# Kernel optimization log

Hardware: AMD Instinct MI355X
Metric: run time of the kernel (lower is better)

The kernel has to match this reference:

```python
import jax, jax.numpy as jnp
import numpy as np
from jax import lax

BN_EPS = 1e-5

def dwconv(x, w, dilation):
    # x: [N,C,H,W], w: [C,1,k,k] depthwise; SAME padding = (r*(k-1)+1)//2
    k = w.shape[-1]
    pad = (dilation * (k - 1) + 1) // 2
    return lax.conv_general_dilated(
        x, w, window_strides=(1, 1), padding=[(pad, pad), (pad, pad)],
        rhs_dilation=(dilation, dilation), feature_group_count=x.shape[1],
        dimension_numbers=('NCHW', 'OIHW', 'NCHW'))

def bn_eval(y, gamma, beta, mean, var):
    # inference BatchNorm2d over channel dim; params: [C]
    inv = gamma * lax.rsqrt(var + BN_EPS)
    return y * inv[None, :, None, None] + (beta - mean * inv)[None, :, None, None]

def setup_inputs() -> dict:
    key = jax.random.key(0)
    ks = jax.random.split(key, 13)
    C = 384
    x = jax.random.normal(ks[0], (16, C, 56, 56), jnp.float32)
    w_lk = jax.random.normal(ks[1], (C, 1, 13, 13), jnp.float32) * 0.05
    w_b0 = jax.random.normal(ks[2], (C, 1, 5, 5), jnp.float32) * 0.05
    w_b1 = jax.random.normal(ks[3], (C, 1, 7, 7), jnp.float32) * 0.05
    w_b2 = jax.random.normal(ks[4], (C, 1, 7, 7), jnp.float32) * 0.05
    w_b3 = jax.random.normal(ks[5], (C, 1, 3, 3), jnp.float32) * 0.05
    w_b4 = jax.random.normal(ks[6], (C, 1, 3, 3), jnp.float32) * 0.05
    w_b5 = jax.random.normal(ks[7], (C, 1, 3, 3), jnp.float32) * 0.05
    bn_gamma = jax.random.uniform(ks[8], (7, C), jnp.float32, 0.5, 1.5)
    bn_beta = jax.random.normal(ks[9], (7, C), jnp.float32) * 0.1
    bn_mean = jax.random.normal(ks[10], (7, C), jnp.float32) * 0.1
    bn_var = jax.random.uniform(ks[11], (7, C), jnp.float32, 0.5, 1.5)
    return dict(x=x, w_lk=w_lk, w_b0=w_b0, w_b1=w_b1, w_b2=w_b2, w_b3=w_b3,
                w_b4=w_b4, w_b5=w_b5, bn_gamma=bn_gamma, bn_beta=bn_beta,
                bn_mean=bn_mean, bn_var=bn_var)

def reference(x, w_lk, w_b0, w_b1, w_b2, w_b3, w_b4, w_b5,
              bn_gamma, bn_beta, bn_mean, bn_var):
    # DilatedReparamBlock (kernel_size=13, non-deploy):
    # out = BN(dw13(x)) + sum_i BN_i(dw_{k_i, r_i}(x))
    dilates = (1, 1, 2, 3, 4, 5)
    branch_ws = (w_b0, w_b1, w_b2, w_b3, w_b4, w_b5)
    out = bn_eval(dwconv(x, w_lk, 1), bn_gamma[0], bn_beta[0], bn_mean[0], bn_var[0])
    for i, (w, r) in enumerate(zip(branch_ws, dilates)):
        j = i + 1
        out = out + bn_eval(dwconv(x, w, r), bn_gamma[j], bn_beta[j], bn_mean[j], bn_var[j])
    return out
```

## Files before the change

### kernel.cpp

```cpp
#include <hip/hip_runtime.h>
#include <hip/hip_fp16.h>


#define CCH 384
#define SP 56
#define PWH 72
#define NPLANES (16*384)

typedef __attribute__((ext_vector_type(4))) unsigned int u32x4;
typedef _Float16 hf2 __attribute__((ext_vector_type(2)));

__device__ __forceinline__ float rfl(float v) {
    return __int_as_float(__builtin_amdgcn_readfirstlane(__float_as_int(v)));
}
__device__ __forceinline__ unsigned rflu(unsigned v) {
    return (unsigned)__builtin_amdgcn_readfirstlane((int)v);
}
__device__ __forceinline__ hf2 as_hf2(unsigned v) {
    union { unsigned u; hf2 h; } x; x.u = v; return x.h;
}
__device__ __forceinline__ float dot2h(float c, unsigned x, unsigned w) {
#if __has_builtin(__builtin_amdgcn_fdot2)
    return __builtin_amdgcn_fdot2(as_hf2(x), as_hf2(w), c, false);
#else
    hf2 xh = as_hf2(x), wh = as_hf2(w);
    return fmaf((float)xh.x, (float)wh.x, fmaf((float)xh.y, (float)wh.y, c));
#endif
}

__global__ __launch_bounds__(64, 2) void drb_conv13_r14(
    const float* __restrict__ x,
    const float* __restrict__ w_lk, const float* __restrict__ w_b0,
    const float* __restrict__ w_b1, const float* __restrict__ w_b2,
    const float* __restrict__ w_b3, const float* __restrict__ w_b4,
    const float* __restrict__ w_b5,
    const float* __restrict__ gamma, const float* __restrict__ beta,
    const float* __restrict__ mean, const float* __restrict__ var,
    float* __restrict__ out)
{
    __shared__ __align__(16) __half sxh[68 * PWH];
    __shared__ __align__(16) float sw[13 * 16];
    __shared__ __align__(16) unsigned swh[13 * 8];

    const int plane = blockIdx.x;
    const int c = plane % CCH;
    const int tid = threadIdx.x;
    const float* __restrict__ xp = x + (size_t)plane * (SP * SP);

    float4 stage[13];
    #pragma unroll
    for (int k = 0; k < 13; k++) {
        int i4 = tid + 64 * k;
        if (i4 < SP * SP / 4) stage[k] = ((const float4*)xp)[i4];
    }

    float S[7];
    float bias = 0.f;
    #pragma unroll
    for (int j = 0; j < 7; j++) {
        float inv = gamma[j * CCH + c] * rsqrtf(var[j * CCH + c] + 1e-5f);
        S[j] = inv;
        bias += beta[j * CCH + c] - mean[j * CCH + c] * inv;
    }

    {
        u32x4 z = {0u, 0u, 0u, 0u};
        #pragma unroll
        for (int k = 0; k < 10; k++) {
            int i = tid + 64 * k;
            if (i < (68 * PWH) / 8) ((u32x4*)sxh)[i] = z;
        }
    }

    #pragma unroll
    for (int k = 0; k < 4; k++) {
        int t = tid + 64 * k;
        if (t < 13 * 16) {
            int ky = t >> 4, kx = t & 15;
            float w = 0.f;
            if (kx < 13) {
                w = S[0] * w_lk[c * 169 + ky * 13 + kx];
                if (ky >= 4 && ky <= 8 && kx >= 4 && kx <= 8)
                    w += S[1] * w_b0[c * 25 + (ky - 4) * 5 + (kx - 4)];
                if (ky >= 3 && ky <= 9 && kx >= 3 && kx <= 9)
                    w += S[2] * w_b1[c * 49 + (ky - 3) * 7 + (kx - 3)];
                if (!(ky & 1) && !(kx & 1))
                    w += S[3] * w_b2[c * 49 + (ky >> 1) * 7 + (kx >> 1)];
                if (ky >= 3 && ky <= 9 && (ky - 3) % 3 == 0 &&
                    kx >= 3 && kx <= 9 && (kx - 3) % 3 == 0)
                    w += S[4] * w_b3[c * 9 + ((ky - 3) / 3) * 3 + (kx - 3) / 3];
                if (ky >= 2 && ky <= 10 && (ky - 2) % 4 == 0 &&
                    kx >= 2 && kx <= 10 && (kx - 2) % 4 == 0)
                    w += S[5] * w_b4[c * 9 + ((ky - 2) / 4) * 3 + (kx - 2) / 4];
                if (ky >= 1 && ky <= 11 && (ky - 1) % 5 == 0 &&
                    kx >= 1 && kx <= 11 && (kx - 1) % 5 == 0)
                    w += S[6] * w_b5[c * 9 + ((ky - 1) / 5) * 3 + (kx - 1) / 5];
            }
            sw[t] = w;
        }
    }

    #pragma unroll
    for (int k = 0; k < 2; k++) {
        int t = tid + 64 * k;
        if (t < 13 * 8) {
            int ky = t >> 3, p = t & 7;
            float w0 = sw[ky * 16 + 2 * p];
            float w1 = sw[ky * 16 + 2 * p + 1];
            hf2 hh; hh.x = (_Float16)w0; hh.y = (_Float16)w1;
            union { hf2 h; unsigned u; } cv; cv.h = hh;
            swh[t] = cv.u;
        }
    }

    #pragma unroll
    for (int k = 0; k < 13; k++) {
        int i4 = tid + 64 * k;
        if (i4 < SP * SP / 4) {
            float4 v = stage[k];
            int r = i4 / 14;
            int col = (i4 - r * 14) * 4;
            __half2* d2 = (__half2*)&sxh[(r + 6) * PWH + col + 8];
            d2[0] = __floats2half2_rn(v.x, v.y);
            d2[1] = __floats2half2_rn(v.z, v.w);
        }
    }
    __syncthreads();

    const int xg = tid & 7;
    const int yg = tid >> 3;
    const int xgc = (xg < 7) ? xg : 3;
    const int Yb = yg * 7;
    const __half* __restrict__ sbaseh = &sxh[Yb * PWH + 8 * xgc];

    float acc[7][8];
    #pragma unroll
    for (int r = 0; r < 7; r++)
        #pragma unroll
        for (int j = 0; j < 8; j++) acc[r][j] = 0.f;

#define ROWDOT(ROWP, DYN, WPA)                                              \
    {                                                                       \
        const u32x4* cp_ = (const u32x4*)(ROWP);                            \
        u32x4 c0_ = cp_[0], c1_ = cp_[1], c2_ = cp_[2];                     \
        unsigned e_[12], o_[11];                                            \
        e_[0]=c0_.x; e_[1]=c0_.y; e_[2]=c0_.z; e_[3]=c0_.w;                 \
        e_[4]=c1_.x; e_[5]=c1_.y; e_[6]=c1_.z; e_[7]=c1_.w;                 \
        e_[8]=c2_.x; e_[9]=c2_.y; e_[10]=c2_.z; e_[11]=c2_.w;               \
        _Pragma("unroll")                                                   \
        for (int t_ = 1; t_ <= 10; t_++)                                    \
            o_[t_] = (e_[t_] >> 16) | (e_[t_ + 1] << 16);                   \
        _Pragma("unroll")                                                   \
        for (int dy_ = 0; dy_ < (DYN); dy_++) {                             \
            const int r_ = i - dy_ - RBASE;                                 \
            if (r_ >= 0 && r_ < 7) {                                        \
                _Pragma("unroll")                                           \
                for (int j_ = 0; j_ < 8; j_++) {                            \
                    float a_ = acc[r_][j_];                                 \
                    _Pragma("unroll")                                       \
                    for (int p_ = 0; p_ < 7; p_++) {                        \
                        unsigned xa_ = (j_ & 1) ? o_[((j_ + 1) >> 1) + p_]  \
                                                : e_[(j_ >> 1) + 1 + p_];   \
                        a_ = dot2h(a_, xa_, WPA[dy_][p_]);                  \
                    }                                                       \
                    acc[r_][j_] = a_;                                       \
                }                                                           \
            }                                                               \
        }                                                                   \
    }

    #pragma unroll 1
    for (int k0 = 0; k0 < 12; k0 += 4) {
        unsigned wp[4][7];
        #pragma unroll
        for (int dy = 0; dy < 4; dy++) {
            const u32x4* wr4 = (const u32x4*)&swh[(k0 + dy) * 8];
            u32x4 A = wr4[0], B = wr4[1];
            wp[dy][0] = rflu(A.x); wp[dy][1] = rflu(A.y);
            wp[dy][2] = rflu(A.z); wp[dy][3] = rflu(A.w);
            wp[dy][4] = rflu(B.x); wp[dy][5] = rflu(B.y);
            wp[dy][6] = rflu(B.z);
        }
        #define RBASE 0
        #pragma unroll
        for (int i = 0; i < 10; i++) {
            const __half* rp = sbaseh + (k0 + i) * PWH;
            ROWDOT(rp, 4, wp)
        }
        #undef RBASE
    }
    {
        unsigned wpT[1][7];
        const u32x4* wr4 = (const u32x4*)&swh[12 * 8];
        u32x4 A = wr4[0], B = wr4[1];
        wpT[0][0] = rflu(A.x); wpT[0][1] = rflu(A.y);
        wpT[0][2] = rflu(A.z); wpT[0][3] = rflu(A.w);
        wpT[0][4] = rflu(B.x); wpT[0][5] = rflu(B.y);
        wpT[0][6] = rflu(B.z);
        #define RBASE 0
        #pragma unroll
        for (int i = 0; i < 7; i++) {
            const __half* rp = sbaseh + (12 + i) * PWH;
            ROWDOT(rp, 1, wpT)
        }
        #undef RBASE
    }
#undef ROWDOT

    if (xg < 7) {
        float* op = out + (size_t)plane * (SP * SP) + Yb * SP + 8 * xg;
        #pragma unroll
        for (int r = 0; r < 7; r++) {
            float4 v0 = make_float4(acc[r][0] + bias, acc[r][1] + bias,
                                    acc[r][2] + bias, acc[r][3] + bias);
            float4 v1 = make_float4(acc[r][4] + bias, acc[r][5] + bias,
                                    acc[r][6] + bias, acc[r][7] + bias);
            *(float4*)(op + r * SP) = v0;
            *(float4*)(op + r * SP + 4) = v1;
        }
    }
}

extern "C" void kernel_launch(void* const* d_in, const int* in_sizes, int n_in,
                              void* d_out, int out_size, void* d_ws, size_t ws_size,
                              hipStream_t stream) {
    const float* x    = (const float*)d_in[0];
    const float* w_lk = (const float*)d_in[1];
    const float* w_b0 = (const float*)d_in[2];
    const float* w_b1 = (const float*)d_in[3];
    const float* w_b2 = (const float*)d_in[4];
    const float* w_b3 = (const float*)d_in[5];
    const float* w_b4 = (const float*)d_in[6];
    const float* w_b5 = (const float*)d_in[7];
    const float* bn_g = (const float*)d_in[8];
    const float* bn_b = (const float*)d_in[9];
    const float* bn_m = (const float*)d_in[10];
    const float* bn_v = (const float*)d_in[11];
    float* out = (float*)d_out;

    drb_conv13_r14<<<dim3(NPLANES), dim3(64), 0, stream>>>(
        x, w_lk, w_b0, w_b1, w_b2, w_b3, w_b4, w_b5,
        bn_g, bn_b, bn_m, bn_v, out);
}
```

Before: 231.1 us.

## Switch inner convolution from fp16 dot2 to packed half2 FMA accumulation

```diff
diff --git a/kernel.cpp b/kernel.cpp
--- a/kernel.cpp
+++ b/kernel.cpp
@@ -8,27 +8,18 @@
 #define NPLANES (16*384)
 
 typedef __attribute__((ext_vector_type(4))) unsigned int u32x4;
-typedef _Float16 hf2 __attribute__((ext_vector_type(2)));
-
-__device__ __forceinline__ float rfl(float v) {
-    return __int_as_float(__builtin_amdgcn_readfirstlane(__float_as_int(v)));
-}
+
 __device__ __forceinline__ unsigned rflu(unsigned v) {
     return (unsigned)__builtin_amdgcn_readfirstlane((int)v);
 }
-__device__ __forceinline__ hf2 as_hf2(unsigned v) {
-    union { unsigned u; hf2 h; } x; x.u = v; return x.h;
-}
-__device__ __forceinline__ float dot2h(float c, unsigned x, unsigned w) {
-#if __has_builtin(__builtin_amdgcn_fdot2)
-    return __builtin_amdgcn_fdot2(as_hf2(x), as_hf2(w), c, false);
-#else
-    hf2 xh = as_hf2(x), wh = as_hf2(w);
-    return fmaf((float)xh.x, (float)wh.x, fmaf((float)xh.y, (float)wh.y, c));
-#endif
-}
-
-__global__ __launch_bounds__(64, 2) void drb_conv13_r14(
+__device__ __forceinline__ __half2 h2(unsigned v) {
+    union { unsigned u; __half2 h; } x; x.u = v; return x.h;
+}
+__device__ __forceinline__ unsigned uh(__half2 h) {
+    union { __half2 h; unsigned u; } x; x.h = h; return x.u;
+}
+
+__global__ __launch_bounds__(64, 2) void drb_conv13_r15(
     const float* __restrict__ x,
     const float* __restrict__ w_lk, const float* __restrict__ w_b0,
     const float* __restrict__ w_b1, const float* __restrict__ w_b2,
@@ -40,7 +31,7 @@
 {
     __shared__ __align__(16) __half sxh[68 * PWH];
     __shared__ __align__(16) float sw[13 * 16];
-    __shared__ __align__(16) unsigned swh[13 * 8];
+    __shared__ __align__(16) unsigned swb[13 * 16];
 
     const int plane = blockIdx.x;
     const int c = plane % CCH;
@@ -101,15 +92,11 @@
     }
 
     #pragma unroll
-    for (int k = 0; k < 2; k++) {
+    for (int k = 0; k < 4; k++) {
         int t = tid + 64 * k;
-        if (t < 13 * 8) {
-            int ky = t >> 3, p = t & 7;
-            float w0 = sw[ky * 16 + 2 * p];
-            float w1 = sw[ky * 16 + 2 * p + 1];
-            hf2 hh; hh.x = (_Float16)w0; hh.y = (_Float16)w1;
-            union { hf2 h; unsigned u; } cv; cv.h = hh;
-            swh[t] = cv.u;
+        if (t < 13 * 16) {
+            float w = sw[t];
+            swb[t] = uh(__floats2half2_rn(w, w));
         }
     }
 
@@ -126,6 +113,7 @@
         }
     }
     __syncthreads();
+    __builtin_amdgcn_s_setprio(1);
 
     const int xg = tid & 7;
     const int yg = tid >> 3;
@@ -139,31 +127,31 @@
         #pragma unroll
         for (int j = 0; j < 8; j++) acc[r][j] = 0.f;
 
-#define ROWDOT(ROWP, DYN, WPA)                                              \
+#define ROWPK(ROWP, DYN)                                                    \
     {                                                                       \
-        const u32x4* cp_ = (const u32x4*)(ROWP);                            \
-        u32x4 c0_ = cp_[0], c1_ = cp_[1], c2_ = cp_[2];                     \
-        unsigned e_[12], o_[11];                                            \
+        const u32x4* cp4_ = (const u32x4*)(ROWP);                           \
+        u32x4 c0_ = cp4_[0], c1_ = cp4_[1], c2_ = cp4_[2];                  \
+        unsigned e_[12], o_[10];                                            \
         e_[0]=c0_.x; e_[1]=c0_.y; e_[2]=c0_.z; e_[3]=c0_.w;                 \
         e_[4]=c1_.x; e_[5]=c1_.y; e_[6]=c1_.z; e_[7]=c1_.w;                 \
         e_[8]=c2_.x; e_[9]=c2_.y; e_[10]=c2_.z; e_[11]=c2_.w;               \
         _Pragma("unroll")                                                   \
-        for (int t_ = 1; t_ <= 10; t_++)                                    \
+        for (int t_ = 1; t_ <= 9; t_++)                                     \
             o_[t_] = (e_[t_] >> 16) | (e_[t_ + 1] << 16);                   \
         _Pragma("unroll")                                                   \
         for (int dy_ = 0; dy_ < (DYN); dy_++) {                             \
-            const int r_ = i - dy_ - RBASE;                                 \
+            const int r_ = i - dy_;                                         \
             if (r_ >= 0 && r_ < 7) {                                        \
                 _Pragma("unroll")                                           \
-                for (int j_ = 0; j_ < 8; j_++) {                            \
-                    float a_ = acc[r_][j_];                                 \
+                for (int cp_ = 0; cp_ < 4; cp_++) {                         \
+                    __half2 hs_ = hacc[r_][cp_];                            \
                     _Pragma("unroll")                                       \
-                    for (int p_ = 0; p_ < 7; p_++) {                        \
-                        unsigned xa_ = (j_ & 1) ? o_[((j_ + 1) >> 1) + p_]  \
-                                                : e_[(j_ >> 1) + 1 + p_];   \
-                        a_ = dot2h(a_, xa_, WPA[dy_][p_]);                  \
+                    for (int kx_ = 0; kx_ < 13; kx_++) {                    \
+                        unsigned xa_ = (kx_ & 1) ? o_[cp_ + ((kx_ + 1) >> 1)] \
+                                                 : e_[cp_ + 1 + (kx_ >> 1)]; \
+                        hs_ = __hfma2(h2(xa_), h2(wbc[dy_][kx_]), hs_);     \
                     }                                                       \
-                    acc[r_][j_] = a_;                                       \
+                    hacc[r_][cp_] = hs_;                                    \
                 }                                                           \
             }                                                               \
         }                                                                   \
@@ -171,41 +159,71 @@
 
     #pragma unroll 1
     for (int k0 = 0; k0 < 12; k0 += 4) {
-        unsigned wp[4][7];
+        unsigned wbc[4][13];
         #pragma unroll
         for (int dy = 0; dy < 4; dy++) {
-            const u32x4* wr4 = (const u32x4*)&swh[(k0 + dy) * 8];
-            u32x4 A = wr4[0], B = wr4[1];
-            wp[dy][0] = rflu(A.x); wp[dy][1] = rflu(A.y);
-            wp[dy][2] = rflu(A.z); wp[dy][3] = rflu(A.w);
-            wp[dy][4] = rflu(B.x); wp[dy][5] = rflu(B.y);
-            wp[dy][6] = rflu(B.z);
-        }
-        #define RBASE 0
+            const u32x4* wr4 = (const u32x4*)&swb[(k0 + dy) * 16];
+            u32x4 A = wr4[0], B = wr4[1], C = wr4[2];
+            wbc[dy][0] = rflu(A.x); wbc[dy][1] = rflu(A.y);
+            wbc[dy][2] = rflu(A.z); wbc[dy][3] = rflu(A.w);
+            wbc[dy][4] = rflu(B.x); wbc[dy][5] = rflu(B.y);
+            wbc[dy][6] = rflu(B.z); wbc[dy][7] = rflu(B.w);
+            wbc[dy][8] = rflu(C.x); wbc[dy][9] = rflu(C.y);
+            wbc[dy][10] = rflu(C.z); wbc[dy][11] = rflu(C.w);
+            wbc[dy][12] = rflu(((const unsigned*)&swb[(k0 + dy) * 16])[12]);
+        }
+        __half2 hacc[7][4];
+        #pragma unroll
+        for (int r = 0; r < 7; r++)
+            #pragma unroll
+            for (int q = 0; q < 4; q++) hacc[r][q] = h2(0u);
         #pragma unroll
         for (int i = 0; i < 10; i++) {
             const __half* rp = sbaseh + (k0 + i) * PWH;
-            ROWDOT(rp, 4, wp)
-        }
-        #undef RBASE
+            ROWPK(rp, 4)
+        }
+        #pragma unroll
+        for (int r = 0; r < 7; r++)
+            #pragma unroll
+            for (int q = 0; q < 4; q++) {
+                float2 f = __half22float2(hacc[r][q]);
+                acc[r][2 * q]     += f.x;
+                acc[r][2 * q + 1] += f.y;
+            }
     }
     {
-        unsigned wpT[1][7];
-        const u32x4* wr4 = (const u32x4*)&swh[12 * 8];
-        u32x4 A = wr4[0], B = wr4[1];
-        wpT[0][0] = rflu(A.x); wpT[0][1] = rflu(A.y);
-        wpT[0][2] = rflu(A.z); wpT[0][3] = rflu(A.w);
-        wpT[0][4] = rflu(B.x); wpT[0][5] = rflu(B.y);
-        wpT[0][6] = rflu(B.z);
-        #define RBASE 0
-        #pragma unroll
-        for (int i = 0; i < 7; i++) {
-            const __half* rp = sbaseh + (12 + i) * PWH;
-            ROWDOT(rp, 1, wpT)
-        }
-        #undef RBASE
-    }
-#undef ROWDOT
+        unsigned wbc[1][13];
+        const u32x4* wr4 = (const u32x4*)&swb[12 * 16];
+        u32x4 A = wr4[0], B = wr4[1], C = wr4[2];
+        wbc[0][0] = rflu(A.x); wbc[0][1] = rflu(A.y);
+        wbc[0][2] = rflu(A.z); wbc[0][3] = rflu(A.w);
+        wbc[0][4] = rflu(B.x); wbc[0][5] = rflu(B.y);
+        wbc[0][6] = rflu(B.z); wbc[0][7] = rflu(B.w);
+        wbc[0][8] = rflu(C.x); wbc[0][9] = rflu(C.y);
+        wbc[0][10] = rflu(C.z); wbc[0][11] = rflu(C.w);
+        wbc[0][12] = rflu(((const unsigned*)&swb[12 * 16])[12]);
+        __half2 hacc[7][4];
+        #pragma unroll
+        for (int r = 0; r < 7; r++)
+            #pragma unroll
+            for (int q = 0; q < 4; q++) hacc[r][q] = h2(0u);
+        #pragma unroll
+        for (int ii = 0; ii < 7; ii++) {
+            const int i = ii;
+            const __half* rp = sbaseh + (12 + ii) * PWH;
+            ROWPK(rp, 1)
+        }
+        #pragma unroll
+        for (int r = 0; r < 7; r++)
+            #pragma unroll
+            for (int q = 0; q < 4; q++) {
+                float2 f = __half22float2(hacc[r][q]);
+                acc[r][2 * q]     += f.x;
+                acc[r][2 * q + 1] += f.y;
+            }
+    }
+#undef ROWPK
+    __builtin_amdgcn_s_setprio(0);
 
     if (xg < 7) {
         float* op = out + (size_t)plane * (SP * SP) + Yb * SP + 8 * xg;
@@ -238,7 +256,7 @@
     const float* bn_v = (const float*)d_in[11];
     float* out = (float*)d_out;
 
-    drb_conv13_r14<<<dim3(NPLANES), dim3(64), 0, stream>>>(
+    drb_conv13_r15<<<dim3(NPLANES), dim3(64), 0, stream>>>(
         x, w_lk, w_b0, w_b1, w_b2, w_b3, w_b4, w_b5,
         bn_g, bn_b, bn_m, bn_v, out);
 }
```

Result: no change. 227.5 us (-1.6%).
